# Kernel tuning notes

Measured on AMD Instinct MI355X. Metric: run time of the kernel, lower is better.

## Reference

```python
import jax, jax.numpy as jnp
import numpy as np

B, S, DM, H, DH = 2, 2048, 2048, 8, 128
INNER = H * DH
ROPE_BASE = 10000.0


def setup_inputs() -> dict:
    key = jax.random.key(0)
    ks = jax.random.split(key, 8)
    sc = 0.02
    return {
        "x": jax.random.normal(ks[0], (B, S, DM), jnp.float32),
        "Wq": jax.random.normal(ks[1], (INNER, DM), jnp.float32) * sc,
        "Wk": jax.random.normal(ks[2], (INNER, DM), jnp.float32) * sc,
        "Wv": jax.random.normal(ks[3], (INNER, DM), jnp.float32) * sc,
        "Wo": jax.random.normal(ks[4], (DM, INNER), jnp.float32) * sc,
        "Wb": jax.random.normal(ks[5], (H, DM), jnp.float32) * sc,
        "bb": jax.random.normal(ks[6], (H,), jnp.float32) * sc,
        "alpha_log": -2.0 + 0.5 * jax.random.normal(ks[7], (H, DH), jnp.float32),
    }


def _rope(t):
    # cos/sin tables of shape [S, DH//2]
    inv_freq = 1.0 / (ROPE_BASE ** (jnp.arange(0, DH, 2, dtype=jnp.float32) / DH))
    freqs = jnp.arange(t, dtype=jnp.float32)[:, None] * inv_freq[None, :]
    return jnp.cos(freqs), jnp.sin(freqs)


def _apply_rotary(x, cos, sin):
    # x: [B,S,H,DH]; cos/sin: [S, DH//2] broadcast over B,H
    x1, x2 = x[..., : DH // 2], x[..., DH // 2 :]
    c = cos[None, :, None, :]
    s = sin[None, :, None, :]
    return jnp.concatenate([x1 * c - x2 * s, x2 * c + x1 * s], axis=-1)


def reference(x, Wq, Wk, Wv, Wo, Wb, bb, alpha_log):
    q = (x @ Wq.T).reshape(B, S, H, DH)
    k = (x @ Wk.T).reshape(B, S, H, DH)
    v = (x @ Wv.T).reshape(B, S, H, DH)

    cos, sin = _rope(S)
    q = _apply_rotary(q, cos, sin)
    k = _apply_rotary(k, cos, sin)

    alpha = jax.nn.sigmoid(alpha_log)                 # [H, DH]
    beta = jax.nn.sigmoid(x @ Wb.T + bb)              # [B, S, H]

    # parallel path: decayed causal linear attention
    qk = jnp.einsum("bshd,bthd->bhst", q, k)          # [B,H,S,S]
    alpha_mean = alpha.mean(axis=-1)                  # [H]
    log_alpha = jnp.log(jnp.clip(alpha_mean, 1e-6))
    pos = jnp.arange(S, dtype=jnp.float32)
    td = pos[:, None] - pos[None, :]                  # [S,S]
    decay_exp = td[None, :, :] * log_alpha[:, None, None]
    decay_exp = jnp.where(td[None, :, :] < 0, -jnp.inf, decay_exp)
    decay = jnp.exp(decay_exp)                        # [B? no: H,S,S]
    weights = qk * decay[None] * beta.transpose(0, 2, 1)[:, :, None, :]
    out = jnp.einsum("bhst,bthe->bshe", weights, v)   # [B,S,H,DH]
    output = out.reshape(B, S, INNER) @ Wo.T          # [B,S,DM]

    # accumulated state (no-grad in original): recurrent scan over time
    alpha_b = alpha[None, :, :, None]                 # [1,H,DH,1]
    kT = jnp.transpose(k, (1, 0, 2, 3))               # [S,B,H,DH]
    vT = jnp.transpose(v, (1, 0, 2, 3))
    bT = jnp.transpose(beta, (1, 0, 2))               # [S,B,H]

    def step(state, inp):
        k_t, v_t, b_t = inp
        kv = jnp.einsum("bhd,bhe->bhde", k_t, v_t)
        state = alpha_b * state + b_t[:, :, None, None] * kv
        return state, None

    state0 = jnp.zeros((B, H, DH, DH), jnp.float32)
    state, _ = jax.lax.scan(step, state0, (kT, vT, bT))
    return output, state
```

## Files before the change

kernel.cpp:

```cpp
#include <hip/hip_runtime.h>
#include <hip/hip_bf16.h>
#include <cstdint>
#include <cstddef>

#define S_LEN 2048
#define DMODEL 2048
#define NHEADS 8
#define DHEAD 128
#define INNER_DIM 1024
#define BATCH 2

typedef __bf16 bf16;
typedef __bf16 bf16x8 __attribute__((ext_vector_type(8)));
typedef __bf16 bf16x4 __attribute__((ext_vector_type(4)));
typedef float f32x4 __attribute__((ext_vector_type(4)));

#define VMCNT(n) asm volatile("s_waitcnt vmcnt(" #n ")" ::: "memory")
#define BAR()                                \
  do {                                       \
    asm volatile("" ::: "memory");           \
    __builtin_amdgcn_s_barrier();            \
    asm volatile("" ::: "memory");           \
  } while (0)

__device__ __forceinline__ void gload_lds16(const void* g, void* l) {
  __builtin_amdgcn_global_load_lds(
      (const __attribute__((address_space(1))) void*)g,
      (__attribute__((address_space(3))) void*)l, 16, 0, 0);
}

__device__ __forceinline__ float sigmoidf_(float x) {
  return 1.0f / (1.0f + expf(-x));
}

__global__ __launch_bounds__(256) void prep_kernel(
    const float* __restrict__ x, const float* __restrict__ wq,
    const float* __restrict__ wk, const float* __restrict__ wv,
    const float* __restrict__ wo, const float* __restrict__ Wb,
    const float* __restrict__ bbias, const float* __restrict__ alpha_log,
    bf16* __restrict__ wqkvb, bf16* __restrict__ wob, bf16* __restrict__ xb,
    float* __restrict__ beta, float* __restrict__ la_mean,
    float* __restrict__ la_d, float2* __restrict__ cs) {
  const int bid = blockIdx.x;
  const int tid = threadIdx.x;

  if (bid < 8192) {
    size_t i4 = ((size_t)bid * 256 + tid) * 4;
    const float* src;
    bf16* dst;
    size_t off;
    if (i4 < 2097152UL)       { src = wq; dst = wqkvb;           off = i4; }
    else if (i4 < 4194304UL)  { src = wk; dst = wqkvb + 2097152; off = i4 - 2097152UL; }
    else if (i4 < 6291456UL)  { src = wv; dst = wqkvb + 4194304; off = i4 - 4194304UL; }
    else                      { src = wo; dst = wob;             off = i4 - 6291456UL; }
    float4 v = *(const float4*)(src + off);
    bf16x4 o;
    o[0] = (bf16)v.x; o[1] = (bf16)v.y; o[2] = (bf16)v.z; o[3] = (bf16)v.w;
    *(bf16x4*)(dst + off) = o;
  } else if (bid < 9216) {
    const int n = (bid - 8192) * 4 + (tid >> 6);
    const int lane = tid & 63;
    float acc[8];
#pragma unroll
    for (int h = 0; h < 8; h++) acc[h] = 0.0f;
    const float4* x4 = (const float4*)(x + (size_t)n * DMODEL);
    bf16* xbr = xb + (size_t)n * DMODEL;
    for (int d4 = lane; d4 < DMODEL / 4; d4 += 64) {
      float4 xv = x4[d4];
      bf16x4 o;
      o[0] = (bf16)xv.x; o[1] = (bf16)xv.y; o[2] = (bf16)xv.z; o[3] = (bf16)xv.w;
      *(bf16x4*)(xbr + d4 * 4) = o;
#pragma unroll
      for (int h = 0; h < 8; h++) {
        float4 wv2 = ((const float4*)(Wb + (size_t)h * DMODEL))[d4];
        acc[h] += xv.x * wv2.x + xv.y * wv2.y + xv.z * wv2.z + xv.w * wv2.w;
      }
    }
#pragma unroll
    for (int off = 32; off; off >>= 1)
#pragma unroll
      for (int h = 0; h < 8; h++) acc[h] += __shfl_down(acc[h], off);
    if (lane == 0) {
#pragma unroll
      for (int h = 0; h < 8; h++)
        beta[(size_t)n * 8 + h] = sigmoidf_(acc[h] + bbias[h]);
    }
  } else if (bid < 9728) {
    int idx = (bid - 9216) * 256 + tid;
    int s = idx >> 6, j = idx & 63;
    float f = (float)s * expf(-(float)j * (9.210340371976184f / 64.0f));
    float sn, c;
    sincosf(f, &sn, &c);
    cs[idx] = make_float2(c, sn);
  } else {
    if (tid >= 64) return;
    const int h = bid - 9728;
    const int lane = tid;
    float a1 = sigmoidf_(alpha_log[h * 128 + lane]);
    float a2 = sigmoidf_(alpha_log[h * 128 + 64 + lane]);
    la_d[h * 128 + lane] = logf(a1);
    la_d[h * 128 + 64 + lane] = logf(a2);
    float s = a1 + a2;
    for (int off = 32; off; off >>= 1) s += __shfl_down(s, off);
    if (lane == 0) la_mean[h] = logf(fmaxf(s * (1.0f / 128.0f), 1e-6f));
  }
}

#define QKV_K 2048
#define QKV_NT 32
#define LSTR 392

__global__ __launch_bounds__(512, 2) void qkv_gemm8p_kernel(
    const bf16* __restrict__ A, const bf16* __restrict__ Bm,
    bf16* __restrict__ C, bf16* __restrict__ vt,
    const float2* __restrict__ cs) {
  __shared__ __align__(16) bf16 smem[2][32768];

  const int id = blockIdx.x;
  const int wg = (id & 7) * 32 + (id >> 3);
  const int tile_n = (wg >> 5) * 384;
  const int tile_m = (wg & 31) * 128;

  const int tid = threadIdx.x;
  const int lane = tid & 63;
  const int w = tid >> 6;
  const int wm = w >> 2;
  const int wn = w & 3;
  const int lr = lane & 15;
  const int kq = lane >> 4;

  const int srow = lane >> 3;
  const int slot = lane & 7;
  const int sgo = (slot ^ srow) * 8;
  const int rloc = w * 8 + srow;

  size_t Aoff[2], Boff[6];
#pragma unroll
  for (int a = 0; a < 2; ++a)
    Aoff[a] = (size_t)(tile_m + a * 64 + rloc) * QKV_K + sgo;
#pragma unroll
  for (int b = 0; b < 6; ++b) {
    const int ldsr = b * 64 + rloc;
    const int qn = ldsr >= 192 ? 1 : 0;
    const int rem = ldsr - qn * 192;
    const int wng = rem / 48;
    const int rr = rem - wng * 48;
    const int gcol = wng * 96 + qn * 48 + rr;
    Boff[b] = (size_t)(tile_n + gcol) * QKV_K + sgo;
  }

  f32x4 acc[4][6];
#pragma unroll
  for (int i = 0; i < 4; i++)
#pragma unroll
    for (int j = 0; j < 6; j++) acc[i][j] = (f32x4){0.f, 0.f, 0.f, 0.f};

  auto stageAA = [&](int buf, int k0) {
#pragma unroll
    for (int a = 0; a < 2; ++a)
      gload_lds16(A + Aoff[a] + k0, &smem[buf][(a * 64 + w * 8) * 64]);
  };
  auto stageB2 = [&](int buf, int k0, int b0) {
#pragma unroll
    for (int u = 0; u < 2; ++u)
      gload_lds16(Bm + Boff[b0 + u] + k0,
                  &smem[buf][8192 + ((b0 + u) * 64 + w * 8) * 64]);
  };

  stageAA(0, 0);
  stageB2(0, 0, 0);
  stageB2(0, 0, 2);
  stageAA(1, 64);
  stageB2(0, 0, 4);
  VMCNT(4);
  BAR();

  for (int t = 0; t < QKV_NT; ++t) {
    const int buf = t & 1;
    const int k0n = (t + 1) * 64;
    const bool h1 = (t + 1 < QKV_NT);
    const bool h2 = (t + 2 < QKV_NT);
    const bf16* ldsA = smem[buf];
    const bf16* ldsB = smem[buf] + 8192;

    bf16x8 af[2][2], b0f[3][2], b1f[3][2];

#pragma unroll
    for (int mi = 0; mi < 2; ++mi)
#pragma unroll
      for (int ks = 0; ks < 2; ++ks)
        af[mi][ks] = *(const bf16x8*)&ldsA[(wm * 64 + mi * 16 + lr) * 64 +
                                           (((ks * 4 + kq) ^ (lr & 7)) * 8)];
#pragma unroll
    for (int ni = 0; ni < 3; ++ni)
#pragma unroll
      for (int ks = 0; ks < 2; ++ks)
        b0f[ni][ks] = *(const bf16x8*)&ldsB[(wn * 48 + ni * 16 + lr) * 64 +
                                            (((ks * 4 + kq) ^ (lr & 7)) * 8)];
    if (h1) stageB2(buf ^ 1, k0n, 0);
    __builtin_amdgcn_s_setprio(1);
#pragma unroll
    for (int mi = 0; mi < 2; ++mi)
#pragma unroll
      for (int ni = 0; ni < 3; ++ni)
#pragma unroll
        for (int ks = 0; ks < 2; ++ks)
          acc[mi][ni] = __builtin_amdgcn_mfma_f32_16x16x32_bf16(
              af[mi][ks], b0f[ni][ks], acc[mi][ni], 0, 0, 0);
    __builtin_amdgcn_s_setprio(0);
    if (h1) VMCNT(4);
    else VMCNT(0);
    BAR();

#pragma unroll
    for (int ni = 0; ni < 3; ++ni)
#pragma unroll
      for (int ks = 0; ks < 2; ++ks)
        b1f[ni][ks] = *(const bf16x8*)&ldsB[(192 + wn * 48 + ni * 16 + lr) * 64 +
                                            (((ks * 4 + kq) ^ (lr & 7)) * 8)];
    if (h1) stageB2(buf ^ 1, k0n, 2);
    __builtin_amdgcn_s_setprio(1);
#pragma unroll
    for (int mi = 0; mi < 2; ++mi)
#pragma unroll
      for (int ni = 0; ni < 3; ++ni)
#pragma unroll
        for (int ks = 0; ks < 2; ++ks)
          acc[mi][3 + ni] = __builtin_amdgcn_mfma_f32_16x16x32_bf16(
              af[mi][ks], b1f[ni][ks], acc[mi][3 + ni], 0, 0, 0);
    __builtin_amdgcn_s_setprio(0);
    BAR();

#pragma unroll
    for (int mi = 0; mi < 2; ++mi)
#pragma unroll
      for (int ks = 0; ks < 2; ++ks)
        af[mi][ks] = *(const bf16x8*)&ldsA[(wm * 64 + 32 + mi * 16 + lr) * 64 +
                                           (((ks * 4 + kq) ^ (lr & 7)) * 8)];
    if (h1) stageB2(buf ^ 1, k0n, 4);
    __builtin_amdgcn_s_setprio(1);
#pragma unroll
    for (int mi = 0; mi < 2; ++mi)
#pragma unroll
      for (int ni = 0; ni < 3; ++ni)
#pragma unroll
        for (int ks = 0; ks < 2; ++ks)
          acc[2 + mi][3 + ni] = __builtin_amdgcn_mfma_f32_16x16x32_bf16(
              af[mi][ks], b1f[ni][ks], acc[2 + mi][3 + ni], 0, 0, 0);
    __builtin_amdgcn_s_setprio(0);
    BAR();

    if (h2) stageAA(buf, (t + 2) * 64);
    __builtin_amdgcn_s_setprio(1);
#pragma unroll
    for (int mi = 0; mi < 2; ++mi)
#pragma unroll
      for (int ni = 0; ni < 3; ++ni)
#pragma unroll
        for (int ks = 0; ks < 2; ++ks)
          acc[2 + mi][ni] = __builtin_amdgcn_mfma_f32_16x16x32_bf16(
              af[mi][ks], b0f[ni][ks], acc[2 + mi][ni], 0, 0, 0);
    __builtin_amdgcn_s_setprio(0);
    if (h1) {
      if (h2) VMCNT(4);
      else VMCNT(2);
    }
    BAR();
  }

  bf16* Ls = &smem[0][0];
  const int rb = kq * 4;
  const bool anyrope = tile_n < 2048;

  if (anyrope) {
#pragma unroll
    for (int mi = 0; mi < 4; ++mi) {
      const int rowL = wm * 64 + mi * 16 + rb;
#pragma unroll
      for (int ni = 0; ni < 6; ++ni) {
        const int colL = wn * 96 + ni * 16 + lr;
        if (tile_n + colL < 2048) {
#pragma unroll
          for (int r2 = 0; r2 < 4; ++r2)
            Ls[(rowL + r2) * LSTR + colL] = (bf16)acc[mi][ni][r2];
        }
      }
    }
    BAR();
  }

#pragma unroll
  for (int mi = 0; mi < 4; ++mi) {
    const int row0 = tile_m + wm * 64 + mi * 16 + rb;
    const int rowL0 = wm * 64 + mi * 16 + rb;
#pragma unroll
    for (int ni = 0; ni < 6; ++ni) {
      const int colL = wn * 96 + ni * 16 + lr;
      const int col = tile_n + colL;
      const int z = col >> 10;
      const int cz = col & 1023;
      bf16* Cz = C + (size_t)z * 4194304UL;
      if (z < 2) {
        const int d = col & 127;
        const int dj = d & 63;
        const bool lohalf = d < 64;
        const int colP = colL + (lohalf ? 64 : -64);
#pragma unroll
        for (int r2 = 0; r2 < 4; ++r2) {
          float own = acc[mi][ni][r2];
          float par = (float)Ls[(rowL0 + r2) * LSTR + colP];
          float2 cv = cs[(size_t)((row0 + r2) & 2047) * 64 + dj];
          float o = lohalf ? (own * cv.x - par * cv.y)
                           : (own * cv.x + par * cv.y);
          Cz[(size_t)(row0 + r2) * 1024 + cz] = (bf16)o;
        }
      } else {
#pragma unroll
        for (int r2 = 0; r2 < 4; ++r2)
          Cz[(size_t)(row0 + r2) * 1024 + cz] = (bf16)acc[mi][ni][r2];
        const int bb2 = row0 >> 11;
        const int ss = row0 & 2047;
        bf16x4 o4;
#pragma unroll
        for (int r2 = 0; r2 < 4; ++r2) o4[r2] = (bf16)acc[mi][ni][r2];
        *(bf16x4*)&vt[(((size_t)bb2 * 8 + (cz >> 7)) * 128 + (cz & 127)) * 2048 +
                      ss] = o4;
      }
    }
  }
}

#define OP_K 1024
#define OP_NT 16

__global__ __launch_bounds__(512, 2) void oproj_kernel(
    const bf16* __restrict__ A, const bf16* __restrict__ Bm,
    float* __restrict__ C) {
  __shared__ __align__(16) bf16 smem[2][24576];

  const int id = blockIdx.x;
  const int wg = (id & 7) * 32 + (id >> 3);
  const int tile_n = (wg >> 5) * 256;
  const int tile_m = (wg & 31) * 128;

  const int tid = threadIdx.x;
  const int lane = tid & 63;
  const int w = tid >> 6;
  const int wm = w >> 2;
  const int wn = w & 3;
  const int lr = lane & 15;
  const int kq = lane >> 4;

  const int srow = lane >> 3;
  const int slot = lane & 7;
  const int sgo = (slot ^ srow) * 8;
  const int rloc = w * 8 + srow;

  size_t Aoff[2], Boff[4];
#pragma unroll
  for (int a = 0; a < 2; ++a)
    Aoff[a] = (size_t)(tile_m + a * 64 + rloc) * OP_K + sgo;
#pragma unroll
  for (int b = 0; b < 4; ++b) {
    const int ldsr = b * 64 + rloc;
    const int qn = ldsr >= 128 ? 1 : 0;
    const int rem = ldsr - qn * 128;
    const int wng = rem >> 5;
    const int rr = rem & 31;
    const int gcol = wng * 64 + qn * 32 + rr;
    Boff[b] = (size_t)(tile_n + gcol) * OP_K + sgo;
  }

  f32x4 acc[4][4];
#pragma unroll
  for (int i = 0; i < 4; i++)
#pragma unroll
    for (int j = 0; j < 4; j++) acc[i][j] = (f32x4){0.f, 0.f, 0.f, 0.f};

  auto stageAA = [&](int buf, int k0) {
#pragma unroll
    for (int a = 0; a < 2; ++a)
      gload_lds16(A + Aoff[a] + k0, &smem[buf][(a * 64 + w * 8) * 64]);
  };
  auto stageB2 = [&](int buf, int k0, int b0) {
#pragma unroll
    for (int u = 0; u < 2; ++u)
      gload_lds16(Bm + Boff[b0 + u] + k0,
                  &smem[buf][8192 + ((b0 + u) * 64 + w * 8) * 64]);
  };

  stageAA(0, 0);
  stageB2(0, 0, 0);
  stageAA(1, 64);
  stageB2(0, 0, 2);
  VMCNT(4);
  BAR();

  for (int t = 0; t < OP_NT; ++t) {
    const int buf = t & 1;
    const int k0n = (t + 1) * 64;
    const bool h1 = (t + 1 < OP_NT);
    const bool h2 = (t + 2 < OP_NT);
    const bf16* ldsA = smem[buf];
    const bf16* ldsB = smem[buf] + 8192;

    bf16x8 af[2][2], b0f[2][2], b1f[2][2];

#pragma unroll
    for (int mi = 0; mi < 2; ++mi)
#pragma unroll
      for (int ks = 0; ks < 2; ++ks)
        af[mi][ks] = *(const bf16x8*)&ldsA[(wm * 64 + mi * 16 + lr) * 64 +
                                           (((ks * 4 + kq) ^ (lr & 7)) * 8)];
#pragma unroll
    for (int ni = 0; ni < 2; ++ni)
#pragma unroll
      for (int ks = 0; ks < 2; ++ks)
        b0f[ni][ks] = *(const bf16x8*)&ldsB[(wn * 32 + ni * 16 + lr) * 64 +
                                            (((ks * 4 + kq) ^ (lr & 7)) * 8)];
    if (h1) stageB2(buf ^ 1, k0n, 0);
    __builtin_amdgcn_s_setprio(1);
#pragma unroll
    for (int mi = 0; mi < 2; ++mi)
#pragma unroll
      for (int ni = 0; ni < 2; ++ni)
#pragma unroll
        for (int ks = 0; ks < 2; ++ks)
          acc[mi][ni] = __builtin_amdgcn_mfma_f32_16x16x32_bf16(
              af[mi][ks], b0f[ni][ks], acc[mi][ni], 0, 0, 0);
    __builtin_amdgcn_s_setprio(0);
    if (h1) VMCNT(4);
    else VMCNT(0);
    BAR();

#pragma unroll
    for (int ni = 0; ni < 2; ++ni)
#pragma unroll
      for (int ks = 0; ks < 2; ++ks)
        b1f[ni][ks] = *(const bf16x8*)&ldsB[(128 + wn * 32 + ni * 16 + lr) * 64 +
                                            (((ks * 4 + kq) ^ (lr & 7)) * 8)];
    if (h1) stageB2(buf ^ 1, k0n, 2);
    __builtin_amdgcn_s_setprio(1);
#pragma unroll
    for (int mi = 0; mi < 2; ++mi)
#pragma unroll
      for (int ni = 0; ni < 2; ++ni)
#pragma unroll
        for (int ks = 0; ks < 2; ++ks)
          acc[mi][2 + ni] = __builtin_amdgcn_mfma_f32_16x16x32_bf16(
              af[mi][ks], b1f[ni][ks], acc[mi][2 + ni], 0, 0, 0);
    __builtin_amdgcn_s_setprio(0);
    BAR();

#pragma unroll
    for (int mi = 0; mi < 2; ++mi)
#pragma unroll
      for (int ks = 0; ks < 2; ++ks)
        af[mi][ks] = *(const bf16x8*)&ldsA[(wm * 64 + 32 + mi * 16 + lr) * 64 +
                                           (((ks * 4 + kq) ^ (lr & 7)) * 8)];
    __builtin_amdgcn_s_setprio(1);
#pragma unroll
    for (int mi = 0; mi < 2; ++mi)
#pragma unroll
      for (int ni = 0; ni < 2; ++ni)
#pragma unroll
        for (int ks = 0; ks < 2; ++ks)
          acc[2 + mi][2 + ni] = __builtin_amdgcn_mfma_f32_16x16x32_bf16(
              af[mi][ks], b1f[ni][ks], acc[2 + mi][2 + ni], 0, 0, 0);
    __builtin_amdgcn_s_setprio(0);
    BAR();

    if (h2) stageAA(buf, (t + 2) * 64);
    __builtin_amdgcn_s_setprio(1);
#pragma unroll
    for (int mi = 0; mi < 2; ++mi)
#pragma unroll
      for (int ni = 0; ni < 2; ++ni)
#pragma unroll
        for (int ks = 0; ks < 2; ++ks)
          acc[2 + mi][ni] = __builtin_amdgcn_mfma_f32_16x16x32_bf16(
              af[mi][ks], b0f[ni][ks], acc[2 + mi][ni], 0, 0, 0);
    __builtin_amdgcn_s_setprio(0);
    if (h1) {
      if (h2) VMCNT(4);
      else VMCNT(2);
    }
    BAR();
  }

  const int rb = kq * 4;
#pragma unroll
  for (int i = 0; i < 4; ++i) {
    const int row0 = tile_m + wm * 64 + (i >> 1) * 32 + (i & 1) * 16 + rb;
#pragma unroll
    for (int j = 0; j < 4; ++j) {
      const int col = tile_n + wn * 64 + (j >> 1) * 32 + (j & 1) * 16 + lr;
#pragma unroll
      for (int r2 = 0; r2 < 4; ++r2)
        C[(size_t)(row0 + r2) * 2048 + col] = acc[i][j][r2];
    }
  }
}

__global__ __launch_bounds__(256) void attn_mfma_kernel(
    const bf16* __restrict__ q, const bf16* __restrict__ k,
    const bf16* __restrict__ vt, const float* __restrict__ beta,
    const float* __restrict__ la_mean, bf16* __restrict__ outb) {
  const int s0 = blockIdx.x * 64;
  const int h = blockIdx.y;
  const int b = blockIdx.z;
  const int tid = threadIdx.x;
  const int w = tid >> 6;
  const int lane = tid & 63;
  const int lr = lane & 15;
  const int kq = lane >> 4;
  const float la = la_mean[h];

  __shared__ __align__(16) bf16 Ps[4][2][16][72];

  const int sg = s0 + w * 16;
  const size_t qbase =
      ((size_t)b * S_LEN + (sg + lr)) * INNER_DIM + h * 128 + kq * 8;
  bf16x8 aq[4];
#pragma unroll
  for (int ks = 0; ks < 4; ks++)
    aq[ks] = *(const bf16x8*)&q[qbase + ks * 32];

  f32x4 O[8];
#pragma unroll
  for (int en = 0; en < 8; en++) O[en] = (f32x4){0.f, 0.f, 0.f, 0.f};

  const size_t kbase = (size_t)b * S_LEN * INNER_DIM + h * 128 + kq * 8;
  const size_t vtbase = ((size_t)b * 8 + h) * 128 * 2048;

#pragma unroll
  for (int tile = 0; tile < 2; tile++) {
    const int tb = s0 - 64 + tile * 64;
    f32x4 sc[4];
#pragma unroll
    for (int nt = 0; nt < 4; nt++) sc[nt] = (f32x4){0.f, 0.f, 0.f, 0.f};
#pragma unroll
    for (int nt = 0; nt < 4; nt++) {
      int t = tb + nt * 16 + lr;
      int tc = t > 0 ? t : 0;
#pragma unroll
      for (int ks = 0; ks < 4; ks++) {
        bf16x8 bk = *(const bf16x8*)&k[kbase + (size_t)tc * INNER_DIM + ks * 32];
        sc[nt] = __builtin_amdgcn_mfma_f32_16x16x32_bf16(aq[ks], bk, sc[nt],
                                                         0, 0, 0);
      }
    }
#pragma unroll
    for (int nt = 0; nt < 4; nt++) {
      int t = tb + nt * 16 + lr;
      int tc = t > 0 ? t : 0;
      float bt = beta[((size_t)b * S_LEN + tc) * 8 + h];
#pragma unroll
      for (int reg = 0; reg < 4; reg++) {
        int qrow = sg + kq * 4 + reg;
        int td = qrow - t;
        float wgt = 0.0f;
        if (t >= 0 && td >= 0 && td < 64)
          wgt = sc[nt][reg] * __expf((float)td * la) * bt;
        Ps[w][tile][kq * 4 + reg][nt * 16 + lr] = (bf16)wgt;
      }
    }
    __syncthreads();
    bf16x8 ap[2];
#pragma unroll
    for (int ks2 = 0; ks2 < 2; ks2++)
      ap[ks2] = *(const bf16x8*)&Ps[w][tile][lr][ks2 * 32 + kq * 8];
#pragma unroll
    for (int en = 0; en < 8; en++) {
#pragma unroll
      for (int ks2 = 0; ks2 < 2; ks2++) {
        int t0f = tb + ks2 * 32 + kq * 8;
        int tcf = t0f > 0 ? t0f : 0;
        bf16x8 bv = *(const bf16x8*)&vt[vtbase + (size_t)(en * 16 + lr) * 2048 +
                                        tcf];
        O[en] = __builtin_amdgcn_mfma_f32_16x16x32_bf16(ap[ks2], bv, O[en], 0,
                                                        0, 0);
      }
    }
  }
  const size_t obase = (size_t)b * S_LEN * INNER_DIM + h * 128;
#pragma unroll
  for (int en = 0; en < 8; en++) {
#pragma unroll
    for (int reg = 0; reg < 4; reg++) {
      int qrow = sg + kq * 4 + reg;
      outb[obase + (size_t)qrow * INNER_DIM + en * 16 + lr] =
          (bf16)O[en][reg];
    }
  }
}

__global__ __launch_bounds__(256) void state_partial_kernel(
    const bf16* __restrict__ k, const bf16* __restrict__ v,
    const float* __restrict__ beta, const float* __restrict__ la_d,
    float* __restrict__ part) {
  const int bh = blockIdx.x;
  const int chunk = blockIdx.y;
  const int b = bh >> 3, h = bh & 7;
  const int t0 = S_LEN - 512 + chunk * 32;
  const int tid = threadIdx.x;
  const int d = tid >> 1;
  const int eh = (tid & 1) * 64;

  __shared__ float ks[32][128];
  __shared__ float vsm[32][128];
  __shared__ float bs[32];

  const size_t bh_off = ((size_t)b * S_LEN) * INNER_DIM + (size_t)h * 128;
  for (int u = tid; u < 32 * 16; u += 256) {
    int r = u >> 4, c8 = (u & 15) * 8;
    bf16x8 kv = *(const bf16x8*)&k[bh_off + (size_t)(t0 + r) * INNER_DIM + c8];
    bf16x8 vv = *(const bf16x8*)&v[bh_off + (size_t)(t0 + r) * INNER_DIM + c8];
#pragma unroll
    for (int j = 0; j < 8; j++) {
      ks[r][c8 + j] = (float)kv[j];
      vsm[r][c8 + j] = (float)vv[j];
    }
  }
  if (tid < 32) bs[tid] = beta[((size_t)b * S_LEN + t0 + tid) * 8 + h];
  __syncthreads();

  const float lad = la_d[h * 128 + d];
  float acc[64];
#pragma unroll
  for (int e = 0; e < 64; e++) acc[e] = 0.0f;

  for (int tl = 0; tl < 32; tl++) {
    int m = (S_LEN - 1) - (t0 + tl);
    float f = __expf((float)m * lad);
    float coef = bs[tl] * ks[tl][d] * f;
    if (coef != 0.0f) {
#pragma unroll
      for (int e = 0; e < 64; e += 4) {
        float4 vv = *(const float4*)&vsm[tl][eh + e];
        acc[e + 0] = fmaf(coef, vv.x, acc[e + 0]);
        acc[e + 1] = fmaf(coef, vv.y, acc[e + 1]);
        acc[e + 2] = fmaf(coef, vv.z, acc[e + 2]);
        acc[e + 3] = fmaf(coef, vv.w, acc[e + 3]);
      }
    }
  }
  float* pp = part + (((size_t)chunk * 16 + bh) * 16384 + (size_t)d * 128 + eh);
#pragma unroll
  for (int e = 0; e < 64; e += 4) {
    float4 o = {acc[e + 0], acc[e + 1], acc[e + 2], acc[e + 3]};
    *(float4*)&pp[e] = o;
  }
}

__global__ __launch_bounds__(256) void state_reduce_kernel(
    const float* __restrict__ part, float* __restrict__ state) {
  size_t off = ((size_t)blockIdx.x * 256 + threadIdx.x) * 4;
  float4 s = {0.f, 0.f, 0.f, 0.f};
#pragma unroll
  for (int c = 0; c < 16; c++) {
    float4 p = *(const float4*)&part[(size_t)c * 262144 + off];
    s.x += p.x; s.y += p.y; s.z += p.z; s.w += p.w;
  }
  *(float4*)&state[off] = s;
}

extern "C" void kernel_launch(void* const* d_in, const int* in_sizes, int n_in,
                              void* d_out, int out_size, void* d_ws,
                              size_t ws_size, hipStream_t stream) {
  const float* x = (const float*)d_in[0];
  const float* Wq = (const float*)d_in[1];
  const float* Wk = (const float*)d_in[2];
  const float* Wv = (const float*)d_in[3];
  const float* Wo = (const float*)d_in[4];
  const float* Wb = (const float*)d_in[5];
  const float* bb = (const float*)d_in[6];
  const float* alog = (const float*)d_in[7];
  float* out = (float*)d_out;

  char* ws = (char*)d_ws;
  bf16* xb = (bf16*)(ws);
  float* part = (float*)(ws);
  bf16* wqkvb = (bf16*)(ws + 16777216UL);
  bf16* wob = (bf16*)(ws + 29360128UL);
  bf16* q = (bf16*)(ws + 33554432UL);
  bf16* kk = (bf16*)(ws + 41943040UL);
  bf16* vv = (bf16*)(ws + 50331648UL);
  bf16* attnb = (bf16*)(ws + 58720256UL);
  bf16* vt = (bf16*)(ws + 67108864UL);
  float* beta = (float*)(ws + 75497472UL);
  float* la_mean = (float*)(ws + 75628544UL);
  float* la_d = (float*)(ws + 75628800UL);
  float2* cs = (float2*)(ws + 75632896UL);

  prep_kernel<<<9736, 256, 0, stream>>>(x, Wq, Wk, Wv, Wo, Wb, bb, alog,
                                        wqkvb, wob, xb, beta, la_mean, la_d,
                                        cs);
  qkv_gemm8p_kernel<<<256, 512, 0, stream>>>(xb, wqkvb, q, vt, cs);
  attn_mfma_kernel<<<dim3(S_LEN / 64, NHEADS, BATCH), 256, 0, stream>>>(
      q, kk, vt, beta, la_mean, attnb);
  state_partial_kernel<<<dim3(16, 16), 256, 0, stream>>>(kk, vv, beta, la_d,
                                                         part);
  state_reduce_kernel<<<256, 256, 0, stream>>>(part, out + 8388608);
  oproj_kernel<<<256, 512, 0, stream>>>(attnb, wob, out);
}
```

Measured before the change: 261.1 us.

## Fold state reduction into oproj launch and narrow attention key window per wave

The state_reduce kernel is removed. Its work runs in 128 extra blocks appended to the oproj launch, which saves one kernel launch and lets the reduction overlap with the GEMM blocks. The attention kernel now gives each wave its own 80-wide key window instead of the shared 128-wide two-tile span. This cuts the QK and PV MFMA work, and the block-wide __syncthreads is replaced by a wave-local lgkmcnt wait. The new code relies on per-wave LDS ordering, adds zero padding for the third PV k-slice, and clamps the V index at the sequence end.

Measured after the change: 257.3 us. No clear change (-1.5%).

```diff
diff --git a/kernel.cpp b/kernel.cpp
--- a/kernel.cpp
+++ b/kernel.cpp
@@ -335,15 +335,28 @@
 
 __global__ __launch_bounds__(512, 2) void oproj_kernel(
     const bf16* __restrict__ A, const bf16* __restrict__ Bm,
-    float* __restrict__ C) {
+    float* __restrict__ C, const float* __restrict__ part) {
   __shared__ __align__(16) bf16 smem[2][24576];
 
   const int id = blockIdx.x;
+  const int tid = threadIdx.x;
+
+  if (id >= 256) {
+    size_t off = (((size_t)id - 256) * 512 + tid) * 4;
+    float4 s = {0.f, 0.f, 0.f, 0.f};
+#pragma unroll
+    for (int c = 0; c < 16; c++) {
+      float4 p = *(const float4*)&part[(size_t)c * 262144 + off];
+      s.x += p.x; s.y += p.y; s.z += p.z; s.w += p.w;
+    }
+    *(float4*)&C[8388608UL + off] = s;
+    return;
+  }
+
   const int wg = (id & 7) * 32 + (id >> 3);
   const int tile_n = (wg >> 5) * 256;
   const int tile_m = (wg & 31) * 128;
 
-  const int tid = threadIdx.x;
   const int lane = tid & 63;
   const int w = tid >> 6;
   const int wm = w >> 2;
@@ -516,9 +529,11 @@
   const int kq = lane >> 4;
   const float la = la_mean[h];
 
-  __shared__ __align__(16) bf16 Ps[4][2][16][72];
+  __shared__ __align__(16) bf16 Ps[4][16][104];
 
   const int sg = s0 + w * 16;
+  const int tb0 = sg - 64;
+
   const size_t qbase =
       ((size_t)b * S_LEN + (sg + lr)) * INNER_DIM + h * 128 + kq * 8;
   bf16x8 aq[4];
@@ -526,63 +541,67 @@
   for (int ks = 0; ks < 4; ks++)
     aq[ks] = *(const bf16x8*)&q[qbase + ks * 32];
 
-  f32x4 O[8];
-#pragma unroll
-  for (int en = 0; en < 8; en++) O[en] = (f32x4){0.f, 0.f, 0.f, 0.f};
-
   const size_t kbase = (size_t)b * S_LEN * INNER_DIM + h * 128 + kq * 8;
   const size_t vtbase = ((size_t)b * 8 + h) * 128 * 2048;
 
-#pragma unroll
-  for (int tile = 0; tile < 2; tile++) {
-    const int tb = s0 - 64 + tile * 64;
-    f32x4 sc[4];
-#pragma unroll
-    for (int nt = 0; nt < 4; nt++) sc[nt] = (f32x4){0.f, 0.f, 0.f, 0.f};
-#pragma unroll
-    for (int nt = 0; nt < 4; nt++) {
-      int t = tb + nt * 16 + lr;
-      int tc = t > 0 ? t : 0;
-#pragma unroll
-      for (int ks = 0; ks < 4; ks++) {
-        bf16x8 bk = *(const bf16x8*)&k[kbase + (size_t)tc * INNER_DIM + ks * 32];
-        sc[nt] = __builtin_amdgcn_mfma_f32_16x16x32_bf16(aq[ks], bk, sc[nt],
-                                                         0, 0, 0);
-      }
-    }
-#pragma unroll
-    for (int nt = 0; nt < 4; nt++) {
-      int t = tb + nt * 16 + lr;
-      int tc = t > 0 ? t : 0;
-      float bt = beta[((size_t)b * S_LEN + tc) * 8 + h];
-#pragma unroll
-      for (int reg = 0; reg < 4; reg++) {
-        int qrow = sg + kq * 4 + reg;
-        int td = qrow - t;
-        float wgt = 0.0f;
-        if (t >= 0 && td >= 0 && td < 64)
-          wgt = sc[nt][reg] * __expf((float)td * la) * bt;
-        Ps[w][tile][kq * 4 + reg][nt * 16 + lr] = (bf16)wgt;
-      }
-    }
-    __syncthreads();
-    bf16x8 ap[2];
-#pragma unroll
-    for (int ks2 = 0; ks2 < 2; ks2++)
-      ap[ks2] = *(const bf16x8*)&Ps[w][tile][lr][ks2 * 32 + kq * 8];
-#pragma unroll
-    for (int en = 0; en < 8; en++) {
-#pragma unroll
-      for (int ks2 = 0; ks2 < 2; ks2++) {
-        int t0f = tb + ks2 * 32 + kq * 8;
-        int tcf = t0f > 0 ? t0f : 0;
-        bf16x8 bv = *(const bf16x8*)&vt[vtbase + (size_t)(en * 16 + lr) * 2048 +
-                                        tcf];
-        O[en] = __builtin_amdgcn_mfma_f32_16x16x32_bf16(ap[ks2], bv, O[en], 0,
-                                                        0, 0);
-      }
-    }
-  }
+  f32x4 sc[5];
+#pragma unroll
+  for (int nt = 0; nt < 5; nt++) sc[nt] = (f32x4){0.f, 0.f, 0.f, 0.f};
+#pragma unroll
+  for (int nt = 0; nt < 5; nt++) {
+    int t = tb0 + nt * 16 + lr;
+    int tc = t > 0 ? t : 0;
+#pragma unroll
+    for (int ks = 0; ks < 4; ks++) {
+      bf16x8 bk = *(const bf16x8*)&k[kbase + (size_t)tc * INNER_DIM + ks * 32];
+      sc[nt] = __builtin_amdgcn_mfma_f32_16x16x32_bf16(aq[ks], bk, sc[nt],
+                                                       0, 0, 0);
+    }
+  }
+
+#pragma unroll
+  for (int nt = 0; nt < 5; nt++) {
+    int t = tb0 + nt * 16 + lr;
+    int tc = t > 0 ? t : 0;
+    float bt = beta[((size_t)b * S_LEN + tc) * 8 + h];
+#pragma unroll
+    for (int reg = 0; reg < 4; reg++) {
+      int qrow = sg + kq * 4 + reg;
+      int td = qrow - t;
+      float wgt = 0.0f;
+      if (t >= 0 && td >= 0 && td < 64)
+        wgt = sc[nt][reg] * __expf((float)td * la) * bt;
+      Ps[w][kq * 4 + reg][nt * 16 + lr] = (bf16)wgt;
+    }
+  }
+#pragma unroll
+  for (int j = 0; j < 4; j++)
+    Ps[w][lr][80 + kq * 4 + j] = (bf16)0.0f;
+
+  asm volatile("s_waitcnt lgkmcnt(0)" ::: "memory");
+  __builtin_amdgcn_sched_barrier(0);
+
+  bf16x8 ap[3];
+#pragma unroll
+  for (int ks2 = 0; ks2 < 3; ks2++)
+    ap[ks2] = *(const bf16x8*)&Ps[w][lr][ks2 * 32 + kq * 8];
+
+  f32x4 O[8];
+#pragma unroll
+  for (int en = 0; en < 8; en++) O[en] = (f32x4){0.f, 0.f, 0.f, 0.f};
+#pragma unroll
+  for (int en = 0; en < 8; en++) {
+#pragma unroll
+    for (int ks2 = 0; ks2 < 3; ks2++) {
+      int t0f = tb0 + ks2 * 32 + kq * 8;
+      int tcf = t0f < 0 ? 0 : (t0f > 2040 ? 2040 : t0f);
+      bf16x8 bv = *(const bf16x8*)&vt[vtbase + (size_t)(en * 16 + lr) * 2048 +
+                                      tcf];
+      O[en] = __builtin_amdgcn_mfma_f32_16x16x32_bf16(ap[ks2], bv, O[en], 0,
+                                                      0, 0);
+    }
+  }
+
   const size_t obase = (size_t)b * S_LEN * INNER_DIM + h * 128;
 #pragma unroll
   for (int en = 0; en < 8; en++) {
@@ -651,18 +670,6 @@
     float4 o = {acc[e + 0], acc[e + 1], acc[e + 2], acc[e + 3]};
     *(float4*)&pp[e] = o;
   }
-}
-
-__global__ __launch_bounds__(256) void state_reduce_kernel(
-    const float* __restrict__ part, float* __restrict__ state) {
-  size_t off = ((size_t)blockIdx.x * 256 + threadIdx.x) * 4;
-  float4 s = {0.f, 0.f, 0.f, 0.f};
-#pragma unroll
-  for (int c = 0; c < 16; c++) {
-    float4 p = *(const float4*)&part[(size_t)c * 262144 + off];
-    s.x += p.x; s.y += p.y; s.z += p.z; s.w += p.w;
-  }
-  *(float4*)&state[off] = s;
 }
 
 extern "C" void kernel_launch(void* const* d_in, const int* in_sizes, int n_in,
@@ -701,6 +708,5 @@
       q, kk, vt, beta, la_mean, attnb);
   state_partial_kernel<<<dim3(16, 16), 256, 0, stream>>>(kk, vv, beta, la_d,
                                                          part);
-  state_reduce_kernel<<<256, 256, 0, stream>>>(part, out + 8388608);
-  oproj_kernel<<<256, 512, 0, stream>>>(attnb, wob, out);
+  oproj_kernel<<<384, 512, 0, stream>>>(attnb, wob, out, part);
 }
```
